# Kernel optimization log

Hardware: AMD Instinct MI355X
Metric: run time of the kernel (lower is better)

The kernel has to match this reference:

```python
import jax, jax.numpy as jnp
import numpy as np

NT, NP, E, H, DIM = 100000, 50000, 800000, 128, 128


def _lin(key, fi, fo):
    k1, k2 = jax.random.split(key)
    w = jax.random.normal(k1, (fi, fo), jnp.float32) * 0.02
    b = jax.random.normal(k2, (fo,), jnp.float32) * 0.02
    return w, b


def _conv_params(key, d_src, d_dst, d_out):
    ks = jax.random.split(key, 5)
    Wq, bq = _lin(ks[0], d_dst, d_out)
    Wk, bk = _lin(ks[1], d_src, d_out)
    Wv, bv = _lin(ks[2], d_src, d_out)
    Ws, bs = _lin(ks[3], d_dst, d_out)
    Wb = jax.random.normal(ks[4], (3 * d_out, 1), jnp.float32) * 0.02
    return Wq, bq, Wk, bk, Wv, bv, Ws, bs, Wb


def setup_inputs() -> dict:
    key = jax.random.key(0)
    ks = jax.random.split(key, 12)
    inp = {}
    inp['x_token'] = jax.random.normal(ks[0], (NT, 1), jnp.float32)
    inp['x_phrase'] = jax.random.normal(ks[1], (NP, H), jnp.float32)
    inp['W_emb'], inp['b_emb'] = _lin(ks[2], 1, H)
    (inp['Wq_tp'], inp['bq_tp'], inp['Wk_tp'], inp['bk_tp'], inp['Wv_tp'],
     inp['bv_tp'], inp['Ws_tp'], inp['bs_tp'], inp['Wb_tp']) = _conv_params(ks[3], H, H, H)
    (inp['Wq_pt'], inp['bq_pt'], inp['Wk_pt'], inp['bk_pt'], inp['Wv_pt'],
     inp['bv_pt'], inp['Ws_pt'], inp['bs_pt'], inp['Wb_pt']) = _conv_params(ks[4], H, H, H)
    inp['W_head'], inp['b_head'] = _lin(ks[5], H, DIM)
    inp['src_tp'] = jax.random.randint(ks[6], (E,), 0, NT, jnp.int32)
    inp['dst_tp'] = jax.random.randint(ks[7], (E,), 0, NP, jnp.int32)
    inp['src_pt'] = jax.random.randint(ks[8], (E,), 0, NP, jnp.int32)
    inp['dst_pt'] = jax.random.randint(ks[9], (E,), 0, NT, jnp.int32)
    return inp


def _tconv(x_src, x_dst, src, dst, Wq, bq, Wk, bk, Wv, bv, Ws, bs, Wb):
    # PyG TransformerConv, heads=1, beta=True, eval mode (no dropout).
    n_dst = x_dst.shape[0]
    d = Wq.shape[1]
    q = x_dst @ Wq + bq          # [Ndst, d]
    k = x_src @ Wk + bk          # [Nsrc, d]
    v = x_src @ Wv + bv          # [Nsrc, d]
    scores = jnp.sum(q[dst] * k[src], axis=-1) / jnp.sqrt(jnp.float32(d))  # [E]
    m = jax.ops.segment_max(scores, dst, num_segments=n_dst)
    m = jnp.where(jnp.isfinite(m), m, 0.0)  # nodes with no in-edges
    e = jnp.exp(scores - m[dst])
    denom = jax.ops.segment_sum(e, dst, num_segments=n_dst)
    alpha = e / (denom[dst] + 1e-16)                       # segment softmax over dst
    out = jax.ops.segment_sum(alpha[:, None] * v[src], dst, num_segments=n_dst)
    skip = x_dst @ Ws + bs
    beta = jax.nn.sigmoid(jnp.concatenate([out, skip, out - skip], axis=-1) @ Wb)
    return beta * skip + (1.0 - beta) * out


def _forward(x_token, x_phrase, W_emb, b_emb,
             Wq_tp, bq_tp, Wk_tp, bk_tp, Wv_tp, bv_tp, Ws_tp, bs_tp, Wb_tp,
             Wq_pt, bq_pt, Wk_pt, bk_pt, Wv_pt, bv_pt, Ws_pt, bs_pt, Wb_pt,
             W_head, b_head, src_tp, dst_tp, src_pt, dst_pt):
    h_t = x_token @ W_emb + b_emb   # [NT, H]
    h_p = x_phrase                  # [NP, H]
    # conv1 (HeteroConv aggr='sum'; each node type has exactly one incoming edge type)
    p1 = _tconv(h_t, h_p, src_tp, dst_tp, Wq_tp, bq_tp, Wk_tp, bk_tp, Wv_tp, bv_tp, Ws_tp, bs_tp, Wb_tp)
    t1 = _tconv(h_p, h_t, src_pt, dst_pt, Wq_pt, bq_pt, Wk_pt, bk_pt, Wv_pt, bv_pt, Ws_pt, bs_pt, Wb_pt)
    p1 = jax.nn.leaky_relu(p1, 0.01)
    t1 = jax.nn.leaky_relu(t1, 0.01)
    # conv2 shares the SAME conv modules (same params). Only the token output is used downstream.
    t2 = _tconv(p1, t1, src_pt, dst_pt, Wq_pt, bq_pt, Wk_pt, bk_pt, Wv_pt, bv_pt, Ws_pt, bs_pt, Wb_pt)
    return t2 @ W_head + b_head     # [NT, DIM]


def reference(x_token, x_phrase, W_emb, b_emb, Wq_tp, bq_tp, Wk_tp, bk_tp, Wv_tp, bv_tp, Ws_tp, bs_tp, Wb_tp, Wq_pt, bq_pt, Wk_pt, bk_pt, Wv_pt, bv_pt, Ws_pt, bs_pt, Wb_pt, W_head, b_head, src_tp, dst_tp, src_pt, dst_pt):
    return _forward(x_token, x_phrase, W_emb, b_emb,
                    Wq_tp, bq_tp, Wk_tp, bk_tp, Wv_tp, bv_tp, Ws_tp, bs_tp, Wb_tp,
                    Wq_pt, bq_pt, Wk_pt, bk_pt, Wv_pt, bv_pt, Ws_pt, bs_pt, Wb_pt,
                    W_head, b_head, src_tp, dst_tp, src_pt, dst_pt)
```

## Files before the change

### kernel.cpp

```cpp
#include <hip/hip_runtime.h>
#include <math.h>

#define NT 100000
#define NP 50000
#define NE 800000
#define H 128
#define NB 196
#define BCAP 8192
#define SPAD 140

#define CDIV(a,b) (((a)+(b)-1)/(b))

typedef __attribute__((ext_vector_type(8))) short s16x8;
typedef __attribute__((ext_vector_type(4))) short s16x4;
typedef __attribute__((ext_vector_type(4))) unsigned short u16x4;
typedef __attribute__((ext_vector_type(4))) float f32x4;

static __device__ __forceinline__ float dot4(float4 a, float4 b){
  return a.x*b.x + a.y*b.y + a.z*b.z + a.w*b.w;
}
static __device__ __forceinline__ float b2f(unsigned short u){
  union { unsigned int i; float f; } c; c.i = ((unsigned int)u) << 16; return c.f;
}
static __device__ __forceinline__ unsigned short f2b(float f){
  union { float f; unsigned int i; } c; c.f = f;
  unsigned int x = c.i;
  unsigned int r = (x + 0x7fffu + ((x >> 16) & 1u)) >> 16;
  return (unsigned short)r;
}
static __device__ __forceinline__ float4 cvt4u(u16x4 h){
  return make_float4(b2f(h[0]), b2f(h[1]), b2f(h[2]), b2f(h[3]));
}

__global__ void kvec4(const float* __restrict__ e, const float* __restrict__ be,
    const float* W0, const float* bi0, float* u0, float* w0,
    const float* W1, const float* bi1, float* u1, float* w1,
    const float* W2, const float* bi2, float* u2, float* w2,
    const float* W3, const float* bi3, float* u3, float* w3){
  const float *W, *bi; float *u, *w;
  switch (blockIdx.x){
    case 0: W=W0; bi=bi0; u=u0; w=w0; break;
    case 1: W=W1; bi=bi1; u=u1; w=w1; break;
    case 2: W=W2; bi=bi2; u=u2; w=w2; break;
    default:W=W3; bi=bi3; u=u3; w=w3; break;
  }
  int j = threadIdx.x;
  float su = 0.f, sw = 0.f;
  for (int i = 0; i < H; ++i) {
    float wv = W[i*H + j];
    su += e[i]*wv;
    sw += be[i]*wv;
  }
  u[j] = su;
  w[j] = sw + bi[j];
}

__global__ void ksetup(const float* __restrict__ Wq, const float* __restrict__ Wk,
                       const float* __restrict__ bq, float* __restrict__ Wqk,
                       float* __restrict__ bqk){
  int i = blockIdx.x;
  int m = threadIdx.x;
  __shared__ float wqr[H];
  wqr[m] = Wq[i*H + m];
  __syncthreads();
  const float* wkr = Wk + m*H;
  float s = 0.f;
  for (int j = 0; j < H; ++j) s += wqr[j] * wkr[j];
  Wqk[i*H + m] = s;
  if (i == 0){
    float t = 0.f;
    for (int j = 0; j < H; ++j) t += bq[j] * wkr[j];
    bqk[m] = t;
  }
}
__global__ void kvqb(const float* __restrict__ Wq, const float* __restrict__ bq,
                     const float* __restrict__ bk, float* __restrict__ vqb,
                     float* __restrict__ c0){
  int i = threadIdx.x;
  float s = 0.f;
  for (int j = 0; j < H; ++j) s += Wq[i*H + j]*bk[j];
  vqb[i] = s;
  if (i == 0){
    float t = 0.f;
    for (int j = 0; j < H; ++j) t += bq[j]*bk[j];
    *c0 = t;
  }
}

__global__ void kprep(const float* W0, unsigned short* P0,
                      const float* W1, unsigned short* P1,
                      const float* W2, unsigned short* P2,
                      const float* W3, unsigned short* P3,
                      const float* W4, unsigned short* P4,
                      const float* W5, unsigned short* P5,
                      const float* W6, unsigned short* P6){
  const float* W; unsigned short* P;
  switch (blockIdx.x){
    case 0: W=W0; P=P0; break;
    case 1: W=W1; P=P1; break;
    case 2: W=W2; P=P2; break;
    case 3: W=W3; P=P3; break;
    case 4: W=W4; P=P4; break;
    case 5: W=W5; P=P5; break;
    default:W=W6; P=P6; break;
  }
  int tid = threadIdx.x;
  for (int it = 0; it < 16; ++it){
    int gid = it*256 + tid;
    int n  = gid & 127;
    int kg = gid >> 7;
    int k0 = kg*4;
    float w0 = W[(k0+0)*H + n];
    float w1 = W[(k0+1)*H + n];
    float w2 = W[(k0+2)*H + n];
    float w3 = W[(k0+3)*H + n];
    unsigned short h0=f2b(w0), h1=f2b(w1), h2=f2b(w2), h3=f2b(w3);
    s16x4 hv; hv[0]=(short)h0; hv[1]=(short)h1; hv[2]=(short)h2; hv[3]=(short)h3;
    s16x4 lv; lv[0]=(short)f2b(w0-b2f(h0)); lv[1]=(short)f2b(w1-b2f(h1));
              lv[2]=(short)f2b(w2-b2f(h2)); lv[3]=(short)f2b(w3-b2f(h3));
    int base = n*128 + (((kg>>1) ^ (n&15))<<3) + ((kg&1)<<2);
    *(s16x4*)(P + base) = hv;
    *(s16x4*)(P + 16384 + base) = lv;
  }
}

static __device__ __forceinline__ void stage_pre32_512(const unsigned short* __restrict__ Wpre,
    unsigned short* __restrict__ WH, int tid){
  const s16x8* src = (const s16x8*)Wpre;
  s16x8 tmp[4];
  #pragma unroll
  for (int it = 0; it < 4; ++it) tmp[it] = src[it*512 + tid];
  #pragma unroll
  for (int it = 0; it < 4; ++it) *(s16x8*)(WH + (it*512 + tid)*8) = tmp[it];
}

static __device__ __forceinline__ void mfma_passW2(const s16x8 AH[4], const s16x8 AL[4],
    const unsigned short* __restrict__ WH, int l15, int l4, f32x4 acc[8]){
  #pragma unroll
  for (int t = 0; t < 8; ++t){ acc[t][0]=0.f; acc[t][1]=0.f; acc[t][2]=0.f; acc[t][3]=0.f; }
  #pragma unroll
  for (int s = 0; s < 4; ++s){
    #pragma unroll
    for (int t = 0; t < 8; ++t){
      int n = t*16 + l15;
      int off = n*128 + (((s*4 + l4) ^ l15)<<3);
      s16x8 BH = *(const s16x8*)(WH + off);
      acc[t] = __builtin_amdgcn_mfma_f32_16x16x32_bf16(AH[s], BH, acc[t], 0,0,0);
      acc[t] = __builtin_amdgcn_mfma_f32_16x16x32_bf16(AL[s], BH, acc[t], 0,0,0);
    }
  }
}
static __device__ __forceinline__ void mfma_passW1(const s16x8 AH[4],
    const unsigned short* __restrict__ WH, int l15, int l4, f32x4 acc[8]){
  #pragma unroll
  for (int t = 0; t < 8; ++t){ acc[t][0]=0.f; acc[t][1]=0.f; acc[t][2]=0.f; acc[t][3]=0.f; }
  #pragma unroll
  for (int s = 0; s < 4; ++s){
    #pragma unroll
    for (int t = 0; t < 8; ++t){
      int n = t*16 + l15;
      int off = n*128 + (((s*4 + l4) ^ l15)<<3);
      s16x8 BH = *(const s16x8*)(WH + off);
      acc[t] = __builtin_amdgcn_mfma_f32_16x16x32_bf16(AH[s], BH, acc[t], 0,0,0);
    }
  }
}

static __device__ __forceinline__ void load_aw_f32(const float* __restrict__ X, int M,
    int rowb, int l15, int l4, s16x8 AH[4], s16x8 AL[4]){
  int row = rowb + l15;
  const float* xr = X + (size_t)row*H;
  bool ok = row < M;
  #pragma unroll
  for (int s = 0; s < 4; ++s){
    int kb = s*32 + l4*8;
    float4 f0 = ok ? *(const float4*)(xr+kb)   : make_float4(0.f,0.f,0.f,0.f);
    float4 f1 = ok ? *(const float4*)(xr+kb+4) : make_float4(0.f,0.f,0.f,0.f);
    float xs[8] = {f0.x,f0.y,f0.z,f0.w,f1.x,f1.y,f1.z,f1.w};
    s16x8 h, lo;
    #pragma unroll
    for (int e = 0; e < 8; ++e){
      unsigned short hh = f2b(xs[e]);
      h[e]  = (short)hh;
      lo[e] = (short)f2b(xs[e] - b2f(hh));
    }
    AH[s] = h; AL[s] = lo;
  }
}
static __device__ __forceinline__ void load_aw_bf16(const unsigned short* __restrict__ Xb, int M,
    int rowb, int l15, int l4, s16x8 AH[4]){
  int row = rowb + l15;
  const unsigned short* xr = Xb + (size_t)row*H;
  bool ok = row < M;
  #pragma unroll
  for (int s = 0; s < 4; ++s){
    s16x8 h = {0,0,0,0,0,0,0,0};
    if (ok) h = *(const s16x8*)(xr + s*32 + l4*8);
    AH[s] = h;
  }
}

static __device__ __forceinline__ void dots_epiW(const f32x4 (&acc)[8],
    const float* __restrict__ bias, const float* __restrict__ uvec,
    const float* __restrict__ wvec, float2* __restrict__ acout,
    int rowb, int M, int l15, int l4){
  float ub[8], wb[8], bb[8];
  #pragma unroll
  for (int t=0;t<8;++t){ ub[t]=uvec[t*16+l15]; wb[t]=wvec[t*16+l15]; bb[t]=bias[t*16+l15]; }
  #pragma unroll
  for (int r=0;r<4;++r){
    float pa=0.f, pc=0.f;
    #pragma unroll
    for (int t=0;t<8;++t){ float y=acc[t][r]+bb[t]; pa+=y*ub[t]; pc+=y*wb[t]; }
    #pragma unroll
    for (int o=1;o<16;o<<=1){ pa+=__shfl_xor(pa,o); pc+=__shfl_xor(pc,o); }
    int row = rowb + l4*4 + r;
    if (l15==0 && row<M) acout[row]=make_float2(pa,pc);
  }
}

static __device__ __forceinline__ void store_cw_bf16(unsigned short* __restrict__ Y,
    const f32x4 (&acc)[8], const float* __restrict__ bias,
    int rowb, int M, int l15, int l4){
  float bb[8];
  #pragma unroll
  for (int t=0;t<8;++t) bb[t]=bias[t*16+l15];
  #pragma unroll
  for (int r=0;r<4;++r){
    int row = rowb + l4*4 + r;
    if (row < M){
      unsigned short* dr = Y + (size_t)row*H;
      #pragma unroll
      for (int t=0;t<8;++t) dr[t*16+l15] = f2b(acc[t][r] + bb[t]);
    }
  }
}
static __device__ __forceinline__ void store_cw_f32(float* __restrict__ Y,
    const f32x4 (&acc)[8], const float* __restrict__ bias,
    int rowb, int M, int l15, int l4){
  float bb[8];
  #pragma unroll
  for (int t=0;t<8;++t) bb[t]=bias[t*16+l15];
  #pragma unroll
  for (int r=0;r<4;++r){
    int row = rowb + l4*4 + r;
    if (row < M){
      float* dr = Y + (size_t)row*H;
      #pragma unroll
      for (int t=0;t<8;++t) dr[t*16+l15] = acc[t][r] + bb[t];
    }
  }
}

__launch_bounds__(512)
__global__ void k_ph(const float* __restrict__ X, int M,
    const unsigned short* __restrict__ WqP, const float* __restrict__ bq,
    const float* __restrict__ uk, const float* __restrict__ wk, float2* __restrict__ ac1,
    const unsigned short* __restrict__ WsP, const float* __restrict__ bs, unsigned short* __restrict__ S1b,
    const unsigned short* __restrict__ WkP, const float* __restrict__ bk,
    const float* __restrict__ uq, const float* __restrict__ wq, float2* __restrict__ ac2,
    const unsigned short* __restrict__ WvP, const float* __restrict__ bv, unsigned short* __restrict__ Vb){
  __shared__ __align__(16) unsigned short WH[16384];
  int tid=threadIdx.x, lane=tid&63, w=tid>>6, l15=lane&15, l4=lane>>4;
  int rowb = blockIdx.x*128 + w*16;

  s16x8 AH[4], AL[4];
  load_aw_f32(X, M, rowb, l15, l4, AH, AL);

  f32x4 acc[8];
  stage_pre32_512(WqP, WH, tid); __syncthreads();
  mfma_passW2(AH, AL, WH, l15, l4, acc);
  __syncthreads();
  dots_epiW(acc, bq, uk, wk, ac1, rowb, M, l15, l4);

  stage_pre32_512(WsP, WH, tid); __syncthreads();
  mfma_passW2(AH, AL, WH, l15, l4, acc);
  __syncthreads();
  store_cw_bf16(S1b, acc, bs, rowb, M, l15, l4);

  stage_pre32_512(WkP, WH, tid); __syncthreads();
  mfma_passW2(AH, AL, WH, l15, l4, acc);
  __syncthreads();
  dots_epiW(acc, bk, uq, wq, ac2, rowb, M, l15, l4);

  stage_pre32_512(WvP, WH, tid); __syncthreads();
  mfma_passW2(AH, AL, WH, l15, l4, acc);
  store_cw_bf16(Vb, acc, bv, rowb, M, l15, l4);
}

__launch_bounds__(512)
__global__ void k_t3f(const unsigned short* __restrict__ T1b, int M,
    const unsigned short* __restrict__ PQK, const float* __restrict__ bqk,
    const float* __restrict__ vqb, const float* __restrict__ c0,
    const unsigned short* __restrict__ PS3, const float* __restrict__ bs3,
    const unsigned short* __restrict__ P1b,
    const int* __restrict__ rowptr, const int* __restrict__ deg,
    const int* __restrict__ srcs,
    const unsigned short* __restrict__ PV2, const float* __restrict__ bv,
    const float* __restrict__ Wb,
    const unsigned short* __restrict__ PHD, const float* __restrict__ bh,
    float* __restrict__ out){
  __shared__ __align__(16) unsigned short WH[16384];
  __shared__ __align__(16) unsigned short SLDS[128][SPAD];
  __shared__ float qbl[128];
  int tid=threadIdx.x, lane=tid&63, w=tid>>6, l15=lane&15, l4=lane>>4;
  int g = tid>>4, gl = tid&15;
  int row0 = blockIdx.x*128;
  int rowb = row0 + w*16;
  const float RS = 0.08838834764831845f;

  s16x8 AH[4];
  load_aw_bf16(T1b, M, rowb, l15, l4, AH);

  {
    float cc0 = *c0;
    float p = 0.f;
    #pragma unroll
    for (int s = 0; s < 4; ++s){
      #pragma unroll
      for (int e = 0; e < 8; ++e)
        p += b2f((unsigned short)AH[s][e]) * vqb[s*32 + l4*8 + e];
    }
    p += __shfl_xor(p, 16);
    p += __shfl_xor(p, 32);
    if (l4 == 0) qbl[w*16 + l15] = p + cc0;
  }

  stage_pre32_512(PQK, WH, tid);
  __syncthreads();
  {
    f32x4 acc[8];
    mfma_passW1(AH, WH, l15, l4, acc);
    float bb[8];
    #pragma unroll
    for (int t=0;t<8;++t) bb[t] = bqk[t*16+l15];
    #pragma unroll
    for (int r=0;r<4;++r){
      int rl = w*16 + l4*4 + r;
      #pragma unroll
      for (int t=0;t<8;++t) SLDS[rl][t*16+l15] = f2b(acc[t][r] + bb[t]);
    }
  }
  __syncthreads();

  stage_pre32_512(PS3, WH, tid);

  #pragma unroll
  for (int tk = 0; tk < 4; ++tk){
    int rl = g*4 + tk;
    int row = row0 + rl;
    if (row < M){
      float q[8];
      {
        s16x8 qh = *(const s16x8*)&SLDS[rl][gl*8];
        #pragma unroll
        for (int e = 0; e < 8; ++e) q[e] = b2f((unsigned short)qh[e]);
      }
      float qb = qbl[rl];
      int rp = rowptr[row], dg = deg[row];
      float d = 0.f;
      float acc8[8] = {0.f,0.f,0.f,0.f,0.f,0.f,0.f,0.f};
      for (int i0 = 0; i0 < dg; i0 += 16){
        int nrem = dg - i0; if (nrem > 16) nrem = 16;
        int mySp = (gl < nrem) ? srcs[rp + i0 + gl] : 0;
        int j = 0;
        for (; j+4 <= nrem; j += 4){
          int sp0 = __shfl(mySp, j, 16),   sp1 = __shfl(mySp, j+1, 16);
          int sp2 = __shfl(mySp, j+2, 16), sp3 = __shfl(mySp, j+3, 16);
          s16x8 h0 = *(const s16x8*)(P1b + (size_t)sp0*H + gl*8);
          s16x8 h1 = *(const s16x8*)(P1b + (size_t)sp1*H + gl*8);
          s16x8 h2 = *(const s16x8*)(P1b + (size_t)sp2*H + gl*8);
          s16x8 h3 = *(const s16x8*)(P1b + (size_t)sp3*H + gl*8);
          float p0[8], p1[8], p2[8], p3[8];
          float ps0 = 0.f, ps1 = 0.f, ps2 = 0.f, ps3 = 0.f;
          #pragma unroll
          for (int e = 0; e < 8; ++e){
            p0[e] = b2f((unsigned short)h0[e]); ps0 += q[e]*p0[e];
            p1[e] = b2f((unsigned short)h1[e]); ps1 += q[e]*p1[e];
            p2[e] = b2f((unsigned short)h2[e]); ps2 += q[e]*p2[e];
            p3[e] = b2f((unsigned short)h3[e]); ps3 += q[e]*p3[e];
          }
          #pragma unroll
          for (int off=1; off<16; off<<=1){
            ps0 += __shfl_xor(ps0,off); ps1 += __shfl_xor(ps1,off);
            ps2 += __shfl_xor(ps2,off); ps3 += __shfl_xor(ps3,off);
          }
          float e0 = __expf((ps0 + qb)*RS), e1 = __expf((ps1 + qb)*RS);
          float e2 = __expf((ps2 + qb)*RS), e3 = __expf((ps3 + qb)*RS);
          d += (e0 + e1) + (e2 + e3);
          #pragma unroll
          for (int e = 0; e < 8; ++e)
            acc8[e] += e0*p0[e] + e1*p1[e] + e2*p2[e] + e3*p3[e];
        }
        for (; j+2 <= nrem; j += 2){
          int spA = __shfl(mySp, j, 16), spB = __shfl(mySp, j+1, 16);
          s16x8 hA = *(const s16x8*)(P1b + (size_t)spA*H + gl*8);
          s16x8 hB = *(const s16x8*)(P1b + (size_t)spB*H + gl*8);
          float pA[8], pB[8];
          float psA = 0.f, psB = 0.f;
          #pragma unroll
          for (int e = 0; e < 8; ++e){
            pA[e] = b2f((unsigned short)hA[e]);
            pB[e] = b2f((unsigned short)hB[e]);
            psA += q[e]*pA[e];
            psB += q[e]*pB[e];
          }
          #pragma unroll
          for (int off=1; off<16; off<<=1){ psA += __shfl_xor(psA,off); psB += __shfl_xor(psB,off); }
          float eA = __expf((psA + qb)*RS), eB = __expf((psB + qb)*RS);
          d += eA + eB;
          #pragma unroll
          for (int e = 0; e < 8; ++e) acc8[e] += eA*pA[e] + eB*pB[e];
        }
        if (j < nrem){
          int sp = __shfl(mySp, j, 16);
          s16x8 h = *(const s16x8*)(P1b + (size_t)sp*H + gl*8);
          float p[8];
          float ps = 0.f;
          #pragma unroll
          for (int e = 0; e < 8; ++e){ p[e] = b2f((unsigned short)h[e]); ps += q[e]*p[e]; }
          #pragma unroll
          for (int off=1; off<16; off<<=1) ps += __shfl_xor(ps,off);
          float ex = __expf((ps + qb)*RS);
          d += ex;
          #pragma unroll
          for (int e = 0; e < 8; ++e) acc8[e] += ex*p[e];
        }
      }
      float inv = 1.f/(d + 1e-16f);
      s16x8 hres;
      #pragma unroll
      for (int e = 0; e < 8; ++e) hres[e] = (short)f2b(acc8[e]*inv);
      *(s16x8*)&SLDS[rl][gl*8] = hres;
    } else {
      s16x8 z = {0,0,0,0,0,0,0,0};
      *(s16x8*)&SLDS[rl][gl*8] = z;
    }
  }
  __syncthreads();

  f32x4 skacc[8];
  mfma_passW1(AH, WH, l15, l4, skacc);
  s16x8 A2[4];
  {
    int rl = w*16 + l15;
    #pragma unroll
    for (int s = 0; s < 4; ++s)
      A2[s] = *(const s16x8*)&SLDS[rl][s*32 + l4*8];
  }
  __syncthreads();

  stage_pre32_512(PV2, WH, tid);
  __syncthreads();

  {
    f32x4 oacc[8];
    mfma_passW1(A2, WH, l15, l4, oacc);
    float bvv[8], bsv[8], wbA[8], wbB[8], wbC[8];
    #pragma unroll
    for (int t = 0; t < 8; ++t){
      int col = t*16 + l15;
      bvv[t] = bv[col]; bsv[t] = bs3[col];
      wbA[t] = Wb[col]; wbB[t] = Wb[H + col]; wbC[t] = Wb[2*H + col];
    }
    #pragma unroll
    for (int r = 0; r < 4; ++r){
      int rl = w*16 + l4*4 + r;
      int row = row0 + rl;
      bool ok = row < M;
      float bsc = (ok && deg[row] > 0) ? 1.f : 0.f;
      float o[8], sk[8];
      float part = 0.f;
      #pragma unroll
      for (int t = 0; t < 8; ++t){
        o[t]  = oacc[t][r] + bvv[t]*bsc;
        sk[t] = skacc[t][r] + bsv[t];
        part += o[t]*wbA[t] + sk[t]*wbB[t] + (o[t]-sk[t])*wbC[t];
      }
      #pragma unroll
      for (int of = 1; of < 16; of <<= 1) part += __shfl_xor(part, of);
      float beta = 1.f/(1.f + __expf(-part));
      #pragma unroll
      for (int t = 0; t < 8; ++t){
        float vv = beta*sk[t] + (1.f-beta)*o[t];
        SLDS[rl][t*16 + l15] = f2b(vv);
      }
    }
  }
  __syncthreads();

  s16x8 A3[4];
  {
    int rl = w*16 + l15;
    #pragma unroll
    for (int s = 0; s < 4; ++s)
      A3[s] = *(const s16x8*)&SLDS[rl][s*32 + l4*8];
  }
  stage_pre32_512(PHD, WH, tid);
  __syncthreads();

  f32x4 hacc[8];
  mfma_passW1(A3, WH, l15, l4, hacc);
  store_cw_f32(out, hacc, bh, rowb, M, l15, l4);
}

template<int GATHER>
__launch_bounds__(256)
__global__ void passA(const int* __restrict__ dst, const int* __restrict__ src,
                      const float* __restrict__ xv, int shift,
                      int* __restrict__ bcnt, int2* __restrict__ out, int n){
  __shared__ int hist[NB];
  __shared__ int base[NB];
  __shared__ int cur[NB];
  int tid = threadIdx.x;
  for (int i = tid; i < NB; i += 256){ hist[i]=0; cur[i]=0; }
  __syncthreads();
  int e0 = blockIdx.x*2048;
  int d[8], s[8];
  #pragma unroll
  for (int k = 0; k < 8; ++k){
    int i = e0 + k*256 + tid;
    if (i < n){ d[k] = dst[i]; s[k] = src[i]; }
    else d[k] = -1;
  }
  #pragma unroll
  for (int k = 0; k < 8; ++k)
    if (d[k] >= 0) atomicAdd(&hist[d[k]>>shift], 1);
  __syncthreads();
  for (int b = tid; b < NB; b += 256)
    base[b] = hist[b] ? atomicAdd(&bcnt[b], hist[b]) : 0;
  __syncthreads();
  #pragma unroll
  for (int k = 0; k < 8; ++k){
    if (d[k] >= 0){
      int b = d[k] >> shift;
      int loc = atomicAdd(&cur[b], 1);
      int2 rec;
      if constexpr (GATHER) rec.x = __float_as_int(xv[s[k]]);
      else                  rec.x = s[k];
      rec.y = d[k] - (b << shift);
      out[(size_t)b*BCAP + base[b] + loc] = rec;
    }
  }
}

__launch_bounds__(512)
__global__ void passB_ph(const int* __restrict__ bcnt, const int2* __restrict__ sorted,
                         const float2* __restrict__ ac, float2* __restrict__ dsv, int np){
  __shared__ float2 acl[256];
  __shared__ float accx[256];
  __shared__ float accy[256];
  int b = blockIdx.x, tid = threadIdx.x;
  int p0 = b*256;
  if (tid < 256){
    int p = p0 + tid;
    acl[tid] = (p < np) ? ac[p] : make_float2(0.f,0.f);
    accx[tid] = 0.f; accy[tid] = 0.f;
  }
  __syncthreads();
  int n = bcnt[b];
  const int2* e = sorted + (size_t)b*BCAP;
  const float RS = 0.08838834764831845f;
  for (int i = tid; i < n; i += 512){
    int2 ed = e[i];
    float x = __int_as_float(ed.x);
    float2 a = acl[ed.y];
    float ex = __expf((x*a.x + a.y)*RS);
    atomicAdd(&accx[ed.y], ex);
    atomicAdd(&accy[ed.y], ex*x);
  }
  __syncthreads();
  if (tid < 256){
    int p = p0 + tid;
    if (p < np) dsv[p] = make_float2(accx[tid], accy[tid]);
  }
}

__launch_bounds__(512)
__global__ void passB_tok(const int* __restrict__ bcnt, const int2* __restrict__ sorted,
                          int* __restrict__ rowptr, int* __restrict__ deg,
                          int* __restrict__ srcs, int ntok){
  __shared__ int cnt[512];
  __shared__ int scn[512];
  __shared__ int cur[512];
  int b = blockIdx.x, tid = threadIdx.x;
  cnt[tid] = 0; cur[tid] = 0;
  __syncthreads();
  int n = bcnt[b];
  const int2* e = sorted + (size_t)b*BCAP;
  for (int i = tid; i < n; i += 512) atomicAdd(&cnt[e[i].y], 1);
  __syncthreads();
  int myc = cnt[tid];
  scn[tid] = myc;
  __syncthreads();
  for (int off = 1; off < 512; off <<= 1){
    int u = (tid >= off) ? scn[tid-off] : 0;
    __syncthreads();
    scn[tid] += u;
    __syncthreads();
  }
  int excl = scn[tid] - myc;
  int tok = b*512 + tid;
  if (tok < ntok){ rowptr[tok] = b*BCAP + excl; deg[tok] = myc; }
  __syncthreads();
  cnt[tid] = excl;
  __syncthreads();
  for (int i = tid; i < n; i += 512){
    int2 ed = e[i];
    int pos = cnt[ed.y] + atomicAdd(&cur[ed.y], 1);
    srcs[(size_t)b*BCAP + pos] = ed.x;
  }
}

template<int OB>
static __device__ __forceinline__ void beta_combine(float4 o, float4 sk,
    const float* __restrict__ Wb, int lane, bool leaky, void* __restrict__ dstRow){
  float4 wb0 = *(const float4*)&Wb[lane*4];
  float4 wb1 = *(const float4*)&Wb[H   + lane*4];
  float4 wb2 = *(const float4*)&Wb[2*H + lane*4];
  float4 dv = make_float4(o.x-sk.x, o.y-sk.y, o.z-sk.z, o.w-sk.w);
  float part = dot4(o,wb0) + dot4(sk,wb1) + dot4(dv,wb2);
  #pragma unroll
  for (int off=1; off<32; off<<=1) part += __shfl_xor(part, off);
  float beta = 1.f/(1.f + __expf(-part));
  float4 r;
  r.x = beta*sk.x + (1.f-beta)*o.x;
  r.y = beta*sk.y + (1.f-beta)*o.y;
  r.z = beta*sk.z + (1.f-beta)*o.z;
  r.w = beta*sk.w + (1.f-beta)*o.w;
  if (leaky){
    r.x = r.x>0.f? r.x : 0.01f*r.x;
    r.y = r.y>0.f? r.y : 0.01f*r.y;
    r.z = r.z>0.f? r.z : 0.01f*r.z;
    r.w = r.w>0.f? r.w : 0.01f*r.w;
  }
  if constexpr (OB){
    ushort4 h; h.x=f2b(r.x); h.y=f2b(r.y); h.z=f2b(r.z); h.w=f2b(r.w);
    *(ushort4*)((unsigned short*)dstRow + lane*4) = h;
  } else {
    *(float4*)((float*)dstRow + lane*4) = r;
  }
}

static __device__ __forceinline__ void beta_combine16(const float o[8], const float sk[8],
    const float* __restrict__ Wb, int lane, bool leaky, unsigned short* __restrict__ dstRow){
  float part = 0.f;
  #pragma unroll
  for (int e = 0; e < 8; ++e){
    int col = lane*8 + e;
    part += o[e]*Wb[col] + sk[e]*Wb[H+col] + (o[e]-sk[e])*Wb[2*H+col];
  }
  #pragma unroll
  for (int off = 1; off < 16; off <<= 1) part += __shfl_xor(part, off);
  float beta = 1.f/(1.f + __expf(-part));
  s16x8 h;
  #pragma unroll
  for (int e = 0; e < 8; ++e){
    float r = beta*sk[e] + (1.f-beta)*o[e];
    if (leaky) r = r > 0.f ? r : 0.01f*r;
    h[e] = (short)f2b(r);
  }
  __builtin_nontemporal_store(h, (s16x8*)(dstRow + lane*8));
}

__global__ void kcomb1(const float2* __restrict__ dsv,
                       const float* __restrict__ uv, const float* __restrict__ wv,
                       const unsigned short* __restrict__ S, const float* __restrict__ Wb,
                       unsigned short* __restrict__ out, int n){
  int gid = (blockIdx.x*blockDim.x + threadIdx.x) >> 5;
  int lane = threadIdx.x & 31;
  if (gid >= n) return;
  float2 ds = dsv[gid];
  float d = ds.x, sv = ds.y;
  float inv = 1.f/(d + 1e-16f);
  float4 u4 = *(const float4*)&uv[lane*4];
  float4 w4 = *(const float4*)&wv[lane*4];
  float4 o = make_float4((sv*u4.x + d*w4.x)*inv, (sv*u4.y + d*w4.y)*inv,
                         (sv*u4.z + d*w4.z)*inv, (sv*u4.w + d*w4.w)*inv);
  u16x4 sh4 = __builtin_nontemporal_load((const u16x4*)(S + (size_t)gid*H + lane*4));
  float4 sk = cvt4u(sh4);
  beta_combine<1>(o, sk, Wb, lane, true, out + (size_t)gid*H);
}

__global__ void knode2(const float* __restrict__ x_tok, const float2* __restrict__ ac,
                       const unsigned short* __restrict__ Vb,
                       const int* __restrict__ rowptr, const int* __restrict__ deg,
                       const int* __restrict__ srcs,
                       const float* __restrict__ us, const float* __restrict__ ws,
                       const float* __restrict__ Wb, unsigned short* __restrict__ out, int n){
  int gid = (blockIdx.x*blockDim.x + threadIdx.x) >> 4;
  int lane = threadIdx.x & 15;
  if (gid >= n) return;
  float xt = x_tok[gid];
  int rp = rowptr[gid], dg = deg[gid];
  const float RS = 0.08838834764831845f;
  float d = 0.f;
  float acc[8] = {0.f,0.f,0.f,0.f,0.f,0.f,0.f,0.f};
  for (int i0 = 0; i0 < dg; i0 += 16){
    int nrem = dg - i0; if (nrem > 16) nrem = 16;
    int mySp = 0; float myE = 0.f;
    if (lane < nrem){
      mySp = srcs[rp + i0 + lane];
      float2 a = ac[mySp];
      myE = __expf((xt*a.x + a.y)*RS);
    }
    float cd = myE;
    #pragma unroll
    for (int of = 1; of < 16; of <<= 1) cd += __shfl_xor(cd, of);
    d += cd;
    int j = 0;
    for (; j+2 <= nrem; j += 2){
      int spA = __shfl(mySp, j, 16),  spB = __shfl(mySp, j+1, 16);
      float eA = __shfl(myE, j, 16),  eB = __shfl(myE, j+1, 16);
      s16x8 hA = *(const s16x8*)(Vb + (size_t)spA*H + lane*8);
      s16x8 hB = *(const s16x8*)(Vb + (size_t)spB*H + lane*8);
      #pragma unroll
      for (int e = 0; e < 8; ++e)
        acc[e] += eA*b2f((unsigned short)hA[e]) + eB*b2f((unsigned short)hB[e]);
    }
    if (j < nrem){
      int sp = __shfl(mySp, j, 16);
      float e0 = __shfl(myE, j, 16);
      s16x8 hv = *(const s16x8*)(Vb + (size_t)sp*H + lane*8);
      #pragma unroll
      for (int e = 0; e < 8; ++e) acc[e] += e0*b2f((unsigned short)hv[e]);
    }
  }
  float inv = 1.f/(d + 1e-16f);
  float o[8], sk[8];
  #pragma unroll
  for (int e = 0; e < 8; ++e){
    int col = lane*8 + e;
    o[e]  = acc[e]*inv;
    sk[e] = xt*us[col] + ws[col];
  }
  beta_combine16(o, sk, Wb, lane, true, out + (size_t)gid*H);
}

extern "C" void kernel_launch(void* const* d_in, const int* in_sizes, int n_in,
                              void* d_out, int out_size, void* d_ws, size_t ws_size,
                              hipStream_t stream){
  const float* x_token  = (const float*)d_in[0];
  const float* x_phrase = (const float*)d_in[1];
  const float* W_emb    = (const float*)d_in[2];
  const float* b_emb    = (const float*)d_in[3];
  const float* Wq_tp = (const float*)d_in[4];  const float* bq_tp = (const float*)d_in[5];
  const float* Wk_tp = (const float*)d_in[6];  const float* bk_tp = (const float*)d_in[7];
  const float* Wv_tp = (const float*)d_in[8];  const float* bv_tp = (const float*)d_in[9];
  const float* Ws_tp = (const float*)d_in[10]; const float* bs_tp = (const float*)d_in[11];
  const float* Wb_tp = (const float*)d_in[12];
  const float* Wq_pt = (const float*)d_in[13]; const float* bq_pt = (const float*)d_in[14];
  const float* Wk_pt = (const float*)d_in[15]; const float* bk_pt = (const float*)d_in[16];
  const float* Wv_pt = (const float*)d_in[17]; const float* bv_pt = (const float*)d_in[18];
  const float* Ws_pt = (const float*)d_in[19]; const float* bs_pt = (const float*)d_in[20];
  const float* Wb_pt = (const float*)d_in[21];
  const float* W_head = (const float*)d_in[22]; const float* b_head = (const float*)d_in[23];
  const int* src_tp = (const int*)d_in[24];
  const int* dst_tp = (const int*)d_in[25];
  const int* src_pt = (const int*)d_in[26];
  const int* dst_pt = (const int*)d_in[27];
  float* out = (float*)d_out;

  char* base = (char*)d_ws;
  size_t off = 0;
  auto AB = [&](size_t bytes)->void*{ void* p=(void*)(base+off); off += (bytes+15)&~(size_t)15; return p; };
  unsigned short* S1b = (unsigned short*)AB((size_t)NP*H*2);
  unsigned short* P1b = (unsigned short*)AB((size_t)NP*H*2);
  unsigned short* Vb  = (unsigned short*)AB((size_t)NP*H*2);
  unsigned short* T1b = (unsigned short*)AB((size_t)NT*H*2);
  float* Wqk = (float*)AB((size_t)H*H*4);
  float* bqk = (float*)AB((size_t)H*4);
  float* vqb = (float*)AB((size_t)H*4);
  float* c0  = (float*)AB(16);
  unsigned short* PQ1 = (unsigned short*)AB(32768*2);
  unsigned short* PS1 = (unsigned short*)AB(32768*2);
  unsigned short* PK2 = (unsigned short*)AB(32768*2);
  unsigned short* PV2 = (unsigned short*)AB(32768*2);
  unsigned short* PS3 = (unsigned short*)AB(32768*2);
  unsigned short* PHD = (unsigned short*)AB(32768*2);
  unsigned short* PQK = (unsigned short*)AB(32768*2);
  float* vecs = (float*)AB(8*H*4);
  float* uk1=vecs, *wk1=vecs+H, *uv1=vecs+2*H, *wv1=vecs+3*H;
  float* uq2=vecs+4*H, *wq2=vecs+5*H, *us2=vecs+6*H, *ws2=vecs+7*H;
  float2* ac1  = (float2*)AB((size_t)NP*8);
  float2* ac2  = (float2*)AB((size_t)NP*8);
  float2* dsv2 = (float2*)AB((size_t)NP*8);
  int2* sortedP = (int2*)AB((size_t)NB*BCAP*8);
  int2* sortedT = (int2*)AB((size_t)NB*BCAP*8);
  int*  srcsT   = (int*)AB((size_t)NB*BCAP*4);
  int* rowT = (int*)AB((size_t)NT*4);
  int* degT = (int*)AB((size_t)NT*4);
  int* bcnt = (int*)AB((size_t)2*NB*4);
  int* bcntP = bcnt, * bcntT = bcnt + NB;
  (void)ws_size; (void)in_sizes; (void)n_in; (void)out_size;

  const int gP = CDIV(NP,128), gT = CDIV(NT,128);
  const int nbA = CDIV(NE,2048);

  kvec4<<<4,H,0,stream>>>(W_emb, b_emb,
      Wk_tp, bk_tp, uk1, wk1,
      Wv_tp, bv_tp, uv1, wv1,
      Wq_pt, bq_pt, uq2, wq2,
      Ws_pt, bs_pt, us2, ws2);
  ksetup<<<H,H,0,stream>>>(Wq_pt, Wk_pt, bq_pt, Wqk, bqk);
  kvqb<<<1,H,0,stream>>>(Wq_pt, bq_pt, bk_pt, vqb, c0);
  kprep<<<7,256,0,stream>>>(Wq_tp, PQ1, Ws_tp, PS1, Wk_pt, PK2, Wv_pt, PV2,
                            Ws_pt, PS3, W_head, PHD, Wqk, PQK);

  (void)hipMemsetAsync(bcnt, 0, (size_t)2*NB*4, stream);
  passA<1><<<nbA,256,0,stream>>>(dst_tp, src_tp, x_token, 8, bcntP, sortedP, NE);
  passA<0><<<nbA,256,0,stream>>>(dst_pt, src_pt, nullptr, 9, bcntT, sortedT, NE);
  passB_tok<<<NB,512,0,stream>>>(bcntT, sortedT, rowT, degT, srcsT, NT);

  k_ph<<<gP,512,0,stream>>>(x_phrase, NP,
      PQ1, bq_tp, uk1, wk1, ac1,
      PS1, bs_tp, S1b,
      PK2, bk_pt, uq2, wq2, ac2,
      PV2, bv_pt, Vb);

  passB_ph<<<NB,512,0,stream>>>(bcntP, sortedP, ac1, dsv2, NP);
  kcomb1<<<CDIV(NP*32,256),256,0,stream>>>(dsv2, uv1, wv1, S1b, Wb_tp, P1b, NP);

  knode2<<<CDIV(NT*16,256),256,0,stream>>>(x_token, ac2, Vb, rowT, degT, srcsT,
                                           us2, ws2, Wb_pt, T1b, NT);

  k_t3f<<<gT,512,0,stream>>>(T1b, NT,
      PQK, bqk, vqb, c0,
      PS3, bs_pt,
      P1b, rowT, degT, srcsT,
      PV2, bv_pt, Wb_pt,
      PHD, b_head, out);
}
```

Baseline: 238.6 us.

## Fuse token aggregation kernel into final conv kernel via shared-memory rows

Removes the separate knode2 kernel that produced T1 token features in global bf16 memory. k_t3f now computes each block's 128 token rows directly (edge softmax over phrase neighbours, V gather, beta gate, leaky ReLU) into LDS, then loads its MFMA A operands from LDS. The PQK weight staging is issued before this aggregation so the two overlap. This saves a launch and the write and read of an NT×H bf16 buffer, but makes the gather-heavy phase share occupancy with the MFMA kernel's large LDS footprint. It also unrolls the gather by four.

```diff
diff --git a/kernel.cpp b/kernel.cpp
--- a/kernel.cpp
+++ b/kernel.cpp
@@ -187,18 +187,6 @@
     AH[s] = h; AL[s] = lo;
   }
 }
-static __device__ __forceinline__ void load_aw_bf16(const unsigned short* __restrict__ Xb, int M,
-    int rowb, int l15, int l4, s16x8 AH[4]){
-  int row = rowb + l15;
-  const unsigned short* xr = Xb + (size_t)row*H;
-  bool ok = row < M;
-  #pragma unroll
-  for (int s = 0; s < 4; ++s){
-    s16x8 h = {0,0,0,0,0,0,0,0};
-    if (ok) h = *(const s16x8*)(xr + s*32 + l4*8);
-    AH[s] = h;
-  }
-}
 
 static __device__ __forceinline__ void dots_epiW(const f32x4 (&acc)[8],
     const float* __restrict__ bias, const float* __restrict__ uvec,
@@ -289,7 +277,9 @@
 }
 
 __launch_bounds__(512)
-__global__ void k_t3f(const unsigned short* __restrict__ T1b, int M,
+__global__ void k_t3f(const float* __restrict__ x_tok,
+    const float2* __restrict__ ac2, const unsigned short* __restrict__ Vb,
+    const float* __restrict__ us, const float* __restrict__ ws, int M,
     const unsigned short* __restrict__ PQK, const float* __restrict__ bqk,
     const float* __restrict__ vqb, const float* __restrict__ c0,
     const unsigned short* __restrict__ PS3, const float* __restrict__ bs3,
@@ -309,8 +299,96 @@
   int rowb = row0 + w*16;
   const float RS = 0.08838834764831845f;
 
+  stage_pre32_512(PQK, WH, tid);
+
+  #pragma unroll
+  for (int tk = 0; tk < 4; ++tk){
+    int rl = g*4 + tk;
+    int row = row0 + rl;
+    if (row < M){
+      float xt = x_tok[row];
+      int rp = rowptr[row], dg = deg[row];
+      float d = 0.f;
+      float acc8[8] = {0.f,0.f,0.f,0.f,0.f,0.f,0.f,0.f};
+      for (int i0 = 0; i0 < dg; i0 += 16){
+        int nrem = dg - i0; if (nrem > 16) nrem = 16;
+        int mySp = 0; float myE = 0.f;
+        if (gl < nrem){
+          mySp = srcs[rp + i0 + gl];
+          float2 a = ac2[mySp];
+          myE = __expf((xt*a.x + a.y)*RS);
+        }
+        float cd = myE;
+        #pragma unroll
+        for (int of = 1; of < 16; of <<= 1) cd += __shfl_xor(cd, of);
+        d += cd;
+        int j = 0;
+        for (; j+4 <= nrem; j += 4){
+          int sp0 = __shfl(mySp, j, 16),   sp1 = __shfl(mySp, j+1, 16);
+          int sp2 = __shfl(mySp, j+2, 16), sp3 = __shfl(mySp, j+3, 16);
+          float e0 = __shfl(myE, j, 16),   e1 = __shfl(myE, j+1, 16);
+          float e2 = __shfl(myE, j+2, 16), e3 = __shfl(myE, j+3, 16);
+          s16x8 h0 = *(const s16x8*)(Vb + (size_t)sp0*H + gl*8);
+          s16x8 h1 = *(const s16x8*)(Vb + (size_t)sp1*H + gl*8);
+          s16x8 h2 = *(const s16x8*)(Vb + (size_t)sp2*H + gl*8);
+          s16x8 h3 = *(const s16x8*)(Vb + (size_t)sp3*H + gl*8);
+          #pragma unroll
+          for (int e = 0; e < 8; ++e)
+            acc8[e] += e0*b2f((unsigned short)h0[e]) + e1*b2f((unsigned short)h1[e])
+                     + e2*b2f((unsigned short)h2[e]) + e3*b2f((unsigned short)h3[e]);
+        }
+        for (; j+2 <= nrem; j += 2){
+          int spA = __shfl(mySp, j, 16),  spB = __shfl(mySp, j+1, 16);
+          float eA = __shfl(myE, j, 16),  eB = __shfl(myE, j+1, 16);
+          s16x8 hA = *(const s16x8*)(Vb + (size_t)spA*H + gl*8);
+          s16x8 hB = *(const s16x8*)(Vb + (size_t)spB*H + gl*8);
+          #pragma unroll
+          for (int e = 0; e < 8; ++e)
+            acc8[e] += eA*b2f((unsigned short)hA[e]) + eB*b2f((unsigned short)hB[e]);
+        }
+        if (j < nrem){
+          int sp = __shfl(mySp, j, 16);
+          float e0 = __shfl(myE, j, 16);
+          s16x8 hv = *(const s16x8*)(Vb + (size_t)sp*H + gl*8);
+          #pragma unroll
+          for (int e = 0; e < 8; ++e) acc8[e] += e0*b2f((unsigned short)hv[e]);
+        }
+      }
+      float inv = 1.f/(d + 1e-16f);
+      float o8[8], sk8[8];
+      float part = 0.f;
+      #pragma unroll
+      for (int e = 0; e < 8; ++e){
+        int col = gl*8 + e;
+        o8[e] = acc8[e]*inv;
+        sk8[e] = xt*us[col] + ws[col];
+        part += o8[e]*Wb[col] + sk8[e]*Wb[H+col] + (o8[e]-sk8[e])*Wb[2*H+col];
+      }
+      #pragma unroll
+      for (int of = 1; of < 16; of <<= 1) part += __shfl_xor(part, of);
+      float beta = 1.f/(1.f + __expf(-part));
+      s16x8 hres;
+      #pragma unroll
+      for (int e = 0; e < 8; ++e){
+        float r = beta*sk8[e] + (1.f-beta)*o8[e];
+        r = r > 0.f ? r : 0.01f*r;
+        hres[e] = (short)f2b(r);
+      }
+      *(s16x8*)&SLDS[rl][gl*8] = hres;
+    } else {
+      s16x8 z = {0,0,0,0,0,0,0,0};
+      *(s16x8*)&SLDS[rl][gl*8] = z;
+    }
+  }
+  __syncthreads();
+
   s16x8 AH[4];
-  load_aw_bf16(T1b, M, rowb, l15, l4, AH);
+  {
+    int rl = w*16 + l15;
+    #pragma unroll
+    for (int s = 0; s < 4; ++s)
+      AH[s] = *(const s16x8*)&SLDS[rl][s*32 + l4*8];
+  }
 
   {
     float cc0 = *c0;
@@ -326,8 +404,6 @@
     if (l4 == 0) qbl[w*16 + l15] = p + cc0;
   }
 
-  stage_pre32_512(PQK, WH, tid);
-  __syncthreads();
   {
     f32x4 acc[8];
     mfma_passW1(AH, WH, l15, l4, acc);
@@ -642,27 +718,6 @@
   }
 }
 
-static __device__ __forceinline__ void beta_combine16(const float o[8], const float sk[8],
-    const float* __restrict__ Wb, int lane, bool leaky, unsigned short* __restrict__ dstRow){
-  float part = 0.f;
-  #pragma unroll
-  for (int e = 0; e < 8; ++e){
-    int col = lane*8 + e;
-    part += o[e]*Wb[col] + sk[e]*Wb[H+col] + (o[e]-sk[e])*Wb[2*H+col];
-  }
-  #pragma unroll
-  for (int off = 1; off < 16; off <<= 1) part += __shfl_xor(part, off);
-  float beta = 1.f/(1.f + __expf(-part));
-  s16x8 h;
-  #pragma unroll
-  for (int e = 0; e < 8; ++e){
-    float r = beta*sk[e] + (1.f-beta)*o[e];
-    if (leaky) r = r > 0.f ? r : 0.01f*r;
-    h[e] = (short)f2b(r);
-  }
-  __builtin_nontemporal_store(h, (s16x8*)(dstRow + lane*8));
-}
-
 __global__ void kcomb1(const float2* __restrict__ dsv,
                        const float* __restrict__ uv, const float* __restrict__ wv,
                        const unsigned short* __restrict__ S, const float* __restrict__ Wb,
@@ -680,61 +735,6 @@
   u16x4 sh4 = __builtin_nontemporal_load((const u16x4*)(S + (size_t)gid*H + lane*4));
   float4 sk = cvt4u(sh4);
   beta_combine<1>(o, sk, Wb, lane, true, out + (size_t)gid*H);
-}
-
-__global__ void knode2(const float* __restrict__ x_tok, const float2* __restrict__ ac,
-                       const unsigned short* __restrict__ Vb,
-                       const int* __restrict__ rowptr, const int* __restrict__ deg,
-                       const int* __restrict__ srcs,
-                       const float* __restrict__ us, const float* __restrict__ ws,
-                       const float* __restrict__ Wb, unsigned short* __restrict__ out, int n){
-  int gid = (blockIdx.x*blockDim.x + threadIdx.x) >> 4;
-  int lane = threadIdx.x & 15;
-  if (gid >= n) return;
-  float xt = x_tok[gid];
-  int rp = rowptr[gid], dg = deg[gid];
-  const float RS = 0.08838834764831845f;
-  float d = 0.f;
-  float acc[8] = {0.f,0.f,0.f,0.f,0.f,0.f,0.f,0.f};
-  for (int i0 = 0; i0 < dg; i0 += 16){
-    int nrem = dg - i0; if (nrem > 16) nrem = 16;
-    int mySp = 0; float myE = 0.f;
-    if (lane < nrem){
-      mySp = srcs[rp + i0 + lane];
-      float2 a = ac[mySp];
-      myE = __expf((xt*a.x + a.y)*RS);
-    }
-    float cd = myE;
-    #pragma unroll
-    for (int of = 1; of < 16; of <<= 1) cd += __shfl_xor(cd, of);
-    d += cd;
-    int j = 0;
-    for (; j+2 <= nrem; j += 2){
-      int spA = __shfl(mySp, j, 16),  spB = __shfl(mySp, j+1, 16);
-      float eA = __shfl(myE, j, 16),  eB = __shfl(myE, j+1, 16);
-      s16x8 hA = *(const s16x8*)(Vb + (size_t)spA*H + lane*8);
-      s16x8 hB = *(const s16x8*)(Vb + (size_t)spB*H + lane*8);
-      #pragma unroll
-      for (int e = 0; e < 8; ++e)
-        acc[e] += eA*b2f((unsigned short)hA[e]) + eB*b2f((unsigned short)hB[e]);
-    }
-    if (j < nrem){
-      int sp = __shfl(mySp, j, 16);
-      float e0 = __shfl(myE, j, 16);
-      s16x8 hv = *(const s16x8*)(Vb + (size_t)sp*H + lane*8);
-      #pragma unroll
-      for (int e = 0; e < 8; ++e) acc[e] += e0*b2f((unsigned short)hv[e]);
-    }
-  }
-  float inv = 1.f/(d + 1e-16f);
-  float o[8], sk[8];
-  #pragma unroll
-  for (int e = 0; e < 8; ++e){
-    int col = lane*8 + e;
-    o[e]  = acc[e]*inv;
-    sk[e] = xt*us[col] + ws[col];
-  }
-  beta_combine16(o, sk, Wb, lane, true, out + (size_t)gid*H);
 }
 
 extern "C" void kernel_launch(void* const* d_in, const int* in_sizes, int n_in,
@@ -767,7 +767,6 @@
   unsigned short* S1b = (unsigned short*)AB((size_t)NP*H*2);
   unsigned short* P1b = (unsigned short*)AB((size_t)NP*H*2);
   unsigned short* Vb  = (unsigned short*)AB((size_t)NP*H*2);
-  unsigned short* T1b = (unsigned short*)AB((size_t)NT*H*2);
   float* Wqk = (float*)AB((size_t)H*H*4);
   float* bqk = (float*)AB((size_t)H*4);
   float* vqb = (float*)AB((size_t)H*4);
@@ -821,10 +820,8 @@
   passB_ph<<<NB,512,0,stream>>>(bcntP, sortedP, ac1, dsv2, NP);
   kcomb1<<<CDIV(NP*32,256),256,0,stream>>>(dsv2, uv1, wv1, S1b, Wb_tp, P1b, NP);
 
-  knode2<<<CDIV(NT*16,256),256,0,stream>>>(x_token, ac2, Vb, rowT, degT, srcsT,
-                                           us2, ws2, Wb_pt, T1b, NT);
-
-  k_t3f<<<gT,512,0,stream>>>(T1b, NT,
+  k_t3f<<<gT,512,0,stream>>>(x_token,
+      ac2, Vb, us2, ws2, NT,
       PQK, bqk, vqb, c0,
       PS3, bs_pt,
       P1b, rowT, degT, srcsT,
```

Result: no change. 239.4 us (+0.3%).
